# Optimization experiments

Measured on AMD Instinct MI355X. Metric: run time of the kernel, lower is better.

## Reference

```python
import jax, jax.numpy as jnp
import numpy as np
from jax import lax

NLAT_IN, NLON_IN = 480, 960
NLAT_OUT, NLON_OUT = 721, 1440
KSIZE = 9      # morlet basis: prod(kernel_shape) = 3*3
NNZ = 20       # sparse quadrature entries per output latitude row
C_IN, C_OUT = 32, 32
BATCH = 1


def setup_inputs() -> dict:
    key = jax.random.key(0)
    k1, k2, k3, k4, k5 = jax.random.split(key, 5)
    x = jax.random.normal(k1, (BATCH, C_IN, NLAT_IN, NLON_IN), dtype=jnp.float32)
    weight = jax.random.normal(k2, (C_OUT, C_IN, KSIZE), dtype=jnp.float32) * 0.05
    # sparse DISCO quadrature values (quadrature weights folded in)
    psi_vals = jax.random.uniform(k3, (KSIZE, NLAT_OUT, NNZ), dtype=jnp.float32) / NNZ
    # geodesic neighborhood: latitude rows within +-2 of output row, small lon offsets
    ho = jnp.arange(NLAT_OUT, dtype=jnp.int32)[:, None]
    psi_hi = jnp.clip(ho + jax.random.randint(k4, (NLAT_OUT, NNZ), -2, 3, dtype=jnp.int32), 0, NLAT_OUT - 1)
    psi_dw = jax.random.randint(k5, (NLAT_OUT, NNZ), -10, 11, dtype=jnp.int32) % NLON_OUT
    return {"x": x, "weight": weight, "psi_vals": psi_vals, "psi_hi": psi_hi, "psi_dw": psi_dw}


def _resample_s2(x, h_out, w_out):
    """Bilinear lat interpolation + periodic linear lon interpolation (ResampleS2)."""
    b, c, h, w = x.shape
    # latitude: both grids are linspace(0, pi, nlat) equiangular
    pos_h = jnp.linspace(0.0, float(h - 1), h_out)
    h0 = jnp.clip(jnp.floor(pos_h).astype(jnp.int32), 0, h - 2)
    fh = (pos_h - h0.astype(jnp.float32)).astype(x.dtype)
    x = x[:, :, h0, :] * (1.0 - fh)[None, None, :, None] + x[:, :, h0 + 1, :] * fh[None, None, :, None]
    # longitude: periodic, lon_j = 2*pi*j/nlon
    pos_w = jnp.arange(w_out, dtype=jnp.float32) * (w / w_out)
    w0 = jnp.floor(pos_w).astype(jnp.int32)
    fw = (pos_w - w0.astype(jnp.float32)).astype(x.dtype)
    w0 = w0 % w
    w1 = (w0 + 1) % w
    return x[..., w0] * (1.0 - fw) + x[..., w1] * fw


def _disco_conv(x, weight, psi_vals, psi_hi, psi_dw):
    """Sparse discrete-continuous spherical conv (gather -> basis weight -> channel mix).
    psi is stored for longitude 0 and applied with a periodic longitude shift."""
    b, c, h, w = x.shape  # [B, Cin, 721, 1440]
    o = weight.shape[0]
    wo = jnp.arange(w, dtype=jnp.int32)

    def body(acc, inp):
        v, hi, dw = inp  # v: [K, Hout], hi/dw: [Hout]
        cols = (dw[:, None] + wo[None, :]) % w          # [Hout, W]
        g = x[:, :, hi[:, None], cols]                  # gather -> [B, Cin, Hout, W]
        weff = jnp.einsum("ock,kh->och", weight, v)     # fold basis into channel mix
        return acc + jnp.einsum("och,bchw->bohw", weff, g), None

    acc0 = jnp.zeros((b, o, h, w), dtype=x.dtype)
    scan_in = (jnp.moveaxis(psi_vals, 2, 0), psi_hi.T, psi_dw.T)  # leading axis NNZ
    acc, _ = lax.scan(body, acc0, scan_in)
    return acc


def reference(x, weight, psi_vals, psi_hi, psi_dw):
    x = _resample_s2(x, NLAT_OUT, NLON_OUT)
    return _disco_conv(x, weight, psi_vals, psi_hi, psi_dw)
```

## Files before the change

kernel.cpp:

```cpp
#include <hip/hip_runtime.h>
#include <hip/hip_bf16.h>

#define NLAT_IN  480
#define NLON_IN  960
#define NLAT_OUT 721
#define NLON_OUT 1440
#define KSIZE    9
#define NNZ      20
#define CH       32

typedef __bf16 bf16x8 __attribute__((ext_vector_type(8)));
typedef float  f32x4  __attribute__((ext_vector_type(4)));

__device__ __forceinline__ unsigned short f2bf(float f) {
    unsigned u = __float_as_uint(f);
    u += 0x7fffu + ((u >> 16) & 1u);
    return (unsigned short)(u >> 16);
}

#define W_TILE   180
#define IN_LD4   31
#define LDS_PITCH 129

__global__ __launch_bounds__(256) void resample_kernel(
        const float* __restrict__ x,
        unsigned short* __restrict__ xr) {
    __shared__ float ld[2 * CH * LDS_PITCH];

    int h  = blockIdx.y;
    int bx = blockIdx.x;
    int wb = bx * W_TILE;
    int base_in = bx * (W_TILE * 2 / 3);

    float pos_h = (float)h * (479.0f / 720.0f);
    int h0 = (int)floorf(pos_h);
    if (h0 < 0) h0 = 0;
    if (h0 > NLAT_IN - 2) h0 = NLAT_IN - 2;
    float fh = pos_h - (float)h0;

    const int t = threadIdx.x;
    for (int i = 0; i < 8; ++i) {
        int lin = i * 256 + t;
        if (lin < 2 * CH * IN_LD4) {
            int r   = lin / (CH * IN_LD4);
            int rem = lin - r * (CH * IN_LD4);
            int c   = rem / IN_LD4;
            int j   = rem - c * IN_LD4;
            int src = base_in + 4 * j;
            if (src >= NLON_IN) src -= NLON_IN;
            f32x4 v = *(const f32x4*)(x + ((size_t)c * NLAT_IN + h0 + r) * NLON_IN + src);
            float* dst = ld + (r * CH + c) * LDS_PITCH + 4 * j;
            dst[0] = v.x; dst[1] = v.y; dst[2] = v.z; dst[3] = v.w;
        }
    }
    __syncthreads();

    float ifh = 1.0f - fh;
    for (int i = 0; i < 12; ++i) {
        int d = i * 256 + t;
        if (d >= W_TILE * (CH / 2)) break;
        int w_l   = d >> 4;
        int cpair = d & 15;
        int c = cpair * 2;
        int w = wb + w_l;
        float pos_w = (float)w * ((float)NLON_IN / (float)NLON_OUT);
        int w0 = (int)floorf(pos_w);
        float fw = pos_w - (float)w0;
        int wl0 = w0 - base_in;
        float ifw = 1.0f - fw;

        const float* r0 = ld + c * LDS_PITCH + wl0;
        const float* r1 = r0 + CH * LDS_PITCH;
        float v0 = ifh * (ifw * r0[0] + fw * r0[1]) + fh * (ifw * r1[0] + fw * r1[1]);
        const float* q0 = r0 + LDS_PITCH;
        const float* q1 = r1 + LDS_PITCH;
        float v1 = ifh * (ifw * q0[0] + fw * q0[1]) + fh * (ifw * q1[0] + fw * q1[1]);

        ((unsigned*)xr)[((size_t)h * NLON_OUT + w) * (CH / 2) + cpair] =
            (unsigned)f2bf(v0) | ((unsigned)f2bf(v1) << 16);
    }
}

__global__ __launch_bounds__(256) void weff_kernel(
        const float* __restrict__ weight,
        const float* __restrict__ psi_vals,
        unsigned short* __restrict__ weff) {
    __shared__ float wl[KSIZE * CH * CH];

    const int t = threadIdx.x;
    for (int i = 0; i < 9; ++i) {
        int lin = i * 256 + t;
        if (lin < KSIZE * CH * CH / 4) {
            f32x4 v = *(const f32x4*)(weight + lin * 4);
            float vv[4] = {v.x, v.y, v.z, v.w};
#pragma unroll
            for (int q = 0; q < 4; ++q) {
                int l4 = lin * 4 + q;
                int k  = l4 % KSIZE;
                int occ = l4 / KSIZE;
                wl[(k * CH * CH) + occ - (occ & 31) + (occ & 31)] = 0;
            }
        }
    }
    __syncthreads();
    for (int i = 0; i < 9; ++i) {
        int lin = i * 256 + t;
        if (lin < KSIZE * CH * CH / 4) {
            f32x4 v = *(const f32x4*)(weight + lin * 4);
            float vv[4] = {v.x, v.y, v.z, v.w};
#pragma unroll
            for (int q = 0; q < 4; ++q) {
                int l4 = lin * 4 + q;
                int k  = l4 % KSIZE;
                int occ = l4 / KSIZE;
                wl[k * (CH * CH) + occ] = vv[q];
            }
        }
    }
    __syncthreads();

    int hnz = blockIdx.x * 16 + (t >> 4);
    int cp  = t & 15;
    if (hnz >= NLAT_OUT * NNZ) return;

    float p[KSIZE];
#pragma unroll
    for (int k = 0; k < KSIZE; ++k)
        p[k] = psi_vals[(size_t)k * (NLAT_OUT * NNZ) + hnz];

    unsigned* outp = (unsigned*)weff + (size_t)hnz * (CH * CH / 2) + cp;
#pragma unroll 4
    for (int oc = 0; oc < CH; ++oc) {
        float a0 = 0.f, a1 = 0.f;
        const float* wb = wl + oc * CH + cp * 2;
#pragma unroll
        for (int k = 0; k < KSIZE; ++k) {
            a0 += wb[k * (CH * CH)]     * p[k];
            a1 += wb[k * (CH * CH) + 1] * p[k];
        }
        outp[oc * 16] = (unsigned)f2bf(a0) | ((unsigned)f2bf(a1) << 16);
    }
}

#define HBLK 181

__global__ __launch_bounds__(384) void disco_kernel(
        const unsigned short* __restrict__ xr,
        const unsigned short* __restrict__ weff,
        const int* __restrict__ psi_hi,
        const int* __restrict__ psi_dw,
        float* __restrict__ out) {
    int bid  = blockIdx.x;
    int xcd  = bid & 7;
    int k    = bid >> 3;
    int hblk = xcd * 23 + k / 5;
    int wblk = k % 5;
    if (hblk >= HBLK) return;

    int wave = threadIdx.x >> 6;
    int lane = threadIdx.x & 63;
    int l15  = lane & 15;
    int quad = lane >> 4;
    int c0   = quad * 8;
    int wbase = wblk * 288 + wave * 48;

    for (int j = 0; j < 4; ++j) {
        int h = hblk * 4 + j;
        if (h >= NLAT_OUT) break;

        f32x4 acc[2][3] = {};
        const unsigned short* weff_h = weff + (size_t)h * (NNZ * CH * CH);
        const int* hip_ = psi_hi + h * NNZ;
        const int* dwp  = psi_dw + h * NNZ;

#pragma unroll 2
        for (int nz = 0; nz < NNZ; ++nz) {
            int hi = hip_[nz];
            int dw = dwp[nz];
            const unsigned short* wf = weff_h + nz * (CH * CH);
            bf16x8 a0 = *(const bf16x8*)(wf + l15 * CH + c0);
            bf16x8 a1 = *(const bf16x8*)(wf + (16 + l15) * CH + c0);
            const unsigned short* xrow = xr + (size_t)hi * (NLON_OUT * CH);
#pragma unroll
            for (int s = 0; s < 3; ++s) {
                int w = wbase + s * 16 + l15 + dw;
                if (w >= NLON_OUT) w -= NLON_OUT;
                bf16x8 b = *(const bf16x8*)(xrow + w * CH + c0);
                acc[0][s] = __builtin_amdgcn_mfma_f32_16x16x32_bf16(a0, b, acc[0][s], 0, 0, 0);
                acc[1][s] = __builtin_amdgcn_mfma_f32_16x16x32_bf16(a1, b, acc[1][s], 0, 0, 0);
            }
        }

#pragma unroll
        for (int hh = 0; hh < 2; ++hh)
#pragma unroll
            for (int s = 0; s < 3; ++s)
#pragma unroll
                for (int r = 0; r < 4; ++r) {
                    int oc = hh * 16 + quad * 4 + r;
                    int w  = wbase + s * 16 + l15;
                    out[((size_t)oc * NLAT_OUT + h) * NLON_OUT + w] = acc[hh][s][r];
                }
    }
}

extern "C" void kernel_launch(void* const* d_in, const int* in_sizes, int n_in,
                              void* d_out, int out_size, void* d_ws, size_t ws_size,
                              hipStream_t stream) {
    const float* x        = (const float*)d_in[0];
    const float* weight   = (const float*)d_in[1];
    const float* psi_vals = (const float*)d_in[2];
    const int*   psi_hi   = (const int*)d_in[3];
    const int*   psi_dw   = (const int*)d_in[4];
    float* out = (float*)d_out;

    unsigned short* xr = (unsigned short*)d_ws;
    unsigned short* wf = (unsigned short*)((char*)d_ws + (size_t)NLAT_OUT * NLON_OUT * CH * 2);

    {
        dim3 grid(NLON_OUT / W_TILE, NLAT_OUT);
        resample_kernel<<<grid, 256, 0, stream>>>(x, xr);
    }
    {
        int nblk = (NLAT_OUT * NNZ + 15) / 16;
        weff_kernel<<<nblk, 256, 0, stream>>>(weight, psi_vals, wf);
    }
    {
        disco_kernel<<<920, 384, 0, stream>>>(xr, wf, psi_hi, psi_dw, out);
    }
}
```

Baseline: 378.4 us.

## Stage resampled input halo tile in LDS for disco conv gathers

The disco kernel now copies an 8-row by 320-column bf16 halo tile of the resampled input into shared memory with global_load_lds, then reads the B operands for the MFMAs from LDS instead of scattered global loads. The grid is re-mapped to 905 (hblk,wblk) pairs split contiguously per XCD. It also drops a redundant zeroing pass in the weff kernel. The LDS tile is about 160KB, which limits occupancy to one block per CU, and LDS reads with a 64-byte row stride may hit bank conflicts.

```diff
diff --git a/kernel.cpp b/kernel.cpp
--- a/kernel.cpp
+++ b/kernel.cpp
@@ -98,21 +98,6 @@
                 int l4 = lin * 4 + q;
                 int k  = l4 % KSIZE;
                 int occ = l4 / KSIZE;
-                wl[(k * CH * CH) + occ - (occ & 31) + (occ & 31)] = 0;
-            }
-        }
-    }
-    __syncthreads();
-    for (int i = 0; i < 9; ++i) {
-        int lin = i * 256 + t;
-        if (lin < KSIZE * CH * CH / 4) {
-            f32x4 v = *(const f32x4*)(weight + lin * 4);
-            float vv[4] = {v.x, v.y, v.z, v.w};
-#pragma unroll
-            for (int q = 0; q < 4; ++q) {
-                int l4 = lin * 4 + q;
-                int k  = l4 % KSIZE;
-                int occ = l4 / KSIZE;
                 wl[k * (CH * CH) + occ] = vv[q];
             }
         }
@@ -142,7 +127,10 @@
     }
 }
 
-#define HBLK 181
+#define ST_ROWS 8
+#define ST_COLS 320
+#define NPAIR   905
+#define PER_XCD 114
 
 __global__ __launch_bounds__(384) void disco_kernel(
         const unsigned short* __restrict__ xr,
@@ -150,22 +138,43 @@
         const int* __restrict__ psi_hi,
         const int* __restrict__ psi_dw,
         float* __restrict__ out) {
-    int bid  = blockIdx.x;
-    int xcd  = bid & 7;
-    int k    = bid >> 3;
-    int hblk = xcd * 23 + k / 5;
-    int wblk = k % 5;
-    if (hblk >= HBLK) return;
+    __shared__ unsigned short st[ST_ROWS * ST_COLS * CH];
+
+    int bid = blockIdx.x;
+    int xcd = bid & 7;
+    int p   = xcd * PER_XCD + (bid >> 3);
+    if (p >= NPAIR) return;
+    int hblk = p / 5;
+    int wblk = p - hblk * 5;
+    int h0    = hblk * 4;
+    int wbase_blk = wblk * 288;
 
     int wave = threadIdx.x >> 6;
     int lane = threadIdx.x & 63;
     int l15  = lane & 15;
     int quad = lane >> 4;
     int c0   = quad * 8;
-    int wbase = wblk * 288 + wave * 48;
-
+
+    int cstart = wbase_blk - 16;
+    if (cstart < 0) cstart += NLON_OUT;
+    for (int i = wave; i < ST_ROWS * (ST_COLS / 16); i += 6) {
+        int r  = i / (ST_COLS / 16);
+        int ck = i - r * (ST_COLS / 16);
+        int gh = h0 - 2 + r;
+        gh = gh < 0 ? 0 : (gh > NLAT_OUT - 1 ? NLAT_OUT - 1 : gh);
+        int gc = cstart + ck * 16;
+        if (gc >= NLON_OUT) gc -= NLON_OUT;
+        const unsigned short* gp = xr + ((size_t)gh * NLON_OUT + gc) * CH + lane * 8;
+        unsigned short* lp = st + (r * ST_COLS + ck * 16) * CH;
+        __builtin_amdgcn_global_load_lds(
+            (const __attribute__((address_space(1))) void*)gp,
+            (__attribute__((address_space(3))) void*)lp, 16, 0, 0);
+    }
+    __syncthreads();
+
+    int wcol0 = 16 + wave * 48;
     for (int j = 0; j < 4; ++j) {
-        int h = hblk * 4 + j;
+        int h = h0 + j;
         if (h >= NLAT_OUT) break;
 
         f32x4 acc[2][3] = {};
@@ -177,15 +186,16 @@
         for (int nz = 0; nz < NNZ; ++nz) {
             int hi = hip_[nz];
             int dw = dwp[nz];
+            int shift = dw > 720 ? dw - NLON_OUT : dw;
+            int rloc  = hi - h0 + 2;
             const unsigned short* wf = weff_h + nz * (CH * CH);
             bf16x8 a0 = *(const bf16x8*)(wf + l15 * CH + c0);
             bf16x8 a1 = *(const bf16x8*)(wf + (16 + l15) * CH + c0);
-            const unsigned short* xrow = xr + (size_t)hi * (NLON_OUT * CH);
+            const unsigned short* srow = st + (size_t)rloc * (ST_COLS * CH);
+            int cbase = wcol0 + l15 + shift;
 #pragma unroll
             for (int s = 0; s < 3; ++s) {
-                int w = wbase + s * 16 + l15 + dw;
-                if (w >= NLON_OUT) w -= NLON_OUT;
-                bf16x8 b = *(const bf16x8*)(xrow + w * CH + c0);
+                bf16x8 b = *(const bf16x8*)(srow + (cbase + s * 16) * CH + c0);
                 acc[0][s] = __builtin_amdgcn_mfma_f32_16x16x32_bf16(a0, b, acc[0][s], 0, 0, 0);
                 acc[1][s] = __builtin_amdgcn_mfma_f32_16x16x32_bf16(a1, b, acc[1][s], 0, 0, 0);
             }
@@ -198,7 +208,7 @@
 #pragma unroll
                 for (int r = 0; r < 4; ++r) {
                     int oc = hh * 16 + quad * 4 + r;
-                    int w  = wbase + s * 16 + l15;
+                    int w  = wbase_blk + wave * 48 + s * 16 + l15;
                     out[((size_t)oc * NLAT_OUT + h) * NLON_OUT + w] = acc[hh][s][r];
                 }
     }
@@ -226,6 +236,6 @@
         weff_kernel<<<nblk, 256, 0, stream>>>(weight, psi_vals, wf);
     }
     {
-        disco_kernel<<<920, 384, 0, stream>>>(xr, wf, psi_hi, psi_dw, out);
-    }
-}
+        disco_kernel<<<8 * PER_XCD, 384, 0, stream>>>(xr, wf, psi_hi, psi_dw, out);
+    }
+}
```

Measured after the change: 342.0 us. 9.6% less time.
